# Optimization experiments

Measured on AMD Instinct MI355X. Metric: run time of the kernel, lower is better.

The kernel has to match this reference:

```python
import jax, jax.numpy as jnp
import numpy as np

EPS = 1e-7  # K.epsilon()

_LC = np.zeros((3, 3, 3), np.float32)  # Levi-Civita for 1x1->1
_LC[0, 1, 2] = _LC[1, 2, 0] = _LC[2, 0, 1] = 1.0
_LC[0, 2, 1] = _LC[2, 1, 0] = _LC[1, 0, 2] = -1.0


def _ssp(x):
    # shifted softplus: log(0.5*exp(x)+0.5)
    return jnp.log(0.5 * jnp.exp(x) + 0.5)


def _radial(image, w1, b1, w2, b2):
    # Sequential([Dense(32), Dense(feat)]) -- linear Dense layers (no activation)
    return (image @ w1 + b1) @ w2 + b2  # (m, a, b, feat)


def setup_inputs() -> dict:
    key = jax.random.key(0)
    ks = jax.random.split(key, 16)
    M, A, RBF, F, SI, H = 4, 256, 64, 32, 32, 32
    inp = {}
    inp["image"] = jax.random.uniform(ks[0], (M, A, A, RBF), dtype=jnp.float32)
    inp["vectors"] = jax.random.normal(ks[1], (M, A, A, 3), dtype=jnp.float32)
    inp["feat0"] = jax.random.normal(ks[2], (M, A, F, 1), dtype=jnp.float32)
    inp["feat1"] = jax.random.normal(ks[3], (M, A, F, 3), dtype=jnp.float32)
    i = 4
    for rin in (0, 1):
        for fro in (0, 1):
            tag = f"{rin}{fro}"
            inp[f"w1_{tag}"] = jax.random.normal(ks[i], (RBF, H)) / np.sqrt(RBF).astype(np.float32)
            inp[f"b1_{tag}"] = jnp.zeros((H,), jnp.float32)
            i += 1
            inp[f"w2_{tag}"] = jax.random.normal(ks[i], (H, F)) / np.sqrt(np.float32(H))
            inp[f"b2_{tag}"] = jnp.zeros((F,), jnp.float32)
            i += 1
    inp["w_si0"] = jax.random.normal(ks[i], (SI, 2 * F)) / np.sqrt(np.float32(2 * F)); i += 1
    inp["w_si1"] = jax.random.normal(ks[i], (SI, 3 * F)) / np.sqrt(np.float32(3 * F)); i += 1
    inp["b_act0"] = jnp.zeros((SI,), jnp.float32)
    inp["b_act1"] = jnp.zeros((SI,), jnp.float32)
    return inp


def reference(image, vectors, feat0, feat1,
              w1_00, b1_00, w2_00, b2_00,
              w1_01, b1_01, w2_01, b2_01,
              w1_10, b1_10, w2_10, b2_10,
              w1_11, b1_11, w2_11, b2_11,
              w_si0, w_si1, b_act0, b_act1):
    # mask where |r_ab| < eps (self-pairs / padding)
    mask = (jnp.sqrt(jnp.sum(vectors * vectors, axis=-1)) < EPS)[..., None]  # (m,a,b,1)

    def filt0(w1, b1, w2, b2):
        return _radial(image, w1, b1, w2, b2)  # (m,a,b,F), implicit rep index of size 1

    def filt1(w1, b1, w2, b2):
        r = jnp.where(mask, 0.0, _radial(image, w1, b1, w2, b2))  # masked radial
        return vectors[:, :, :, None, :] * r[..., None]  # (m,a,b,F,3)

    f0_in0 = filt0(w1_00, b1_00, w2_00, b2_00)
    f1_in0 = filt1(w1_01, b1_01, w2_01, b2_01)
    f0_in1 = filt0(w1_10, b1_10, w2_10, b2_10)
    f1_in1 = filt1(w1_11, b1_11, w2_11, b2_11)

    # point convolution (sum over neighbor atoms b)
    out_0x0_0 = jnp.einsum('mabf,mbfj->mafj', f0_in0, feat0)   # (m,a,F,1)
    out_0x1_1 = jnp.einsum('mabfi,mbfj->mafi', f1_in0, feat0)  # (m,a,F,3)
    out_1x0_1 = jnp.einsum('mabf,mbfj->mafj', f0_in1, feat1)   # (m,a,F,3)
    cg0 = jnp.eye(3, dtype=image.dtype)[None]                  # (1,3,3): 1x1->0
    out_1x1_0 = jnp.einsum('ijk,mabfj,mbfk->mafi', cg0, f1_in1, feat1)  # (m,a,F,1)
    lc = jnp.asarray(_LC, image.dtype)                         # 1x1->1
    out_1x1_1 = jnp.einsum('ijk,mabfj,mbfk->mafi', lc, f1_in1, feat1)   # (m,a,F,3)

    # concat along channel dim per output RO
    cat0 = jnp.concatenate([out_0x0_0, out_1x1_0], axis=2)  # (m,a,2F,1)
    cat1 = jnp.concatenate([out_0x1_1, out_1x0_1, out_1x1_1], axis=2)  # (m,a,3F,3)

    # self-interaction: einsum('mafi,gf->maig') then transpose -> (m,a,g,i)
    si0 = jnp.einsum('mafi,gf->magi', cat0, w_si0)  # (m,a,SI,1)
    si1 = jnp.einsum('mafi,gf->magi', cat1, w_si1)  # (m,a,SI,3)

    # equivariant activation
    o0 = _ssp(si0 + b_act0[None, None, :, None])
    n1 = jnp.sqrt(jnp.maximum(jnp.sum(si1 * si1, axis=-1), EPS))  # norm_with_epsilon
    a1 = _ssp(n1 + b_act1)
    o1 = si1 * (a1 / n1)[..., None]
    return (o0, o1)
```

## Files before the change

kernel.cpp:

```cpp
#include <hip/hip_runtime.h>
#include <math.h>

#define M_ 4
#define A_ 256
#define RBF_ 64
#define F_ 32
#define H_ 32
#define SI_ 32
#define TF_ 128

typedef __attribute__((ext_vector_type(8))) short bf16x8;
typedef __attribute__((ext_vector_type(4))) float f32x4;
typedef __attribute__((ext_vector_type(3))) float f32x3;

__device__ __forceinline__ unsigned short f2bf(float f) {
  union { float f; unsigned u; } v; v.f = f;
  unsigned r = v.u + 0x7FFFu + ((v.u >> 16) & 1u);
  return (unsigned short)(r >> 16);
}

__device__ __forceinline__ unsigned pack2bf(float lo, float hi) {
  union { float f; unsigned u; } a, b; a.f = lo; b.f = hi;
  return __builtin_amdgcn_perm(b.u + 0x8000u, a.u + 0x8000u, 0x07060302u);
}

__device__ __forceinline__ float sspf(float x) {
  return fmaxf(x, 0.f) + log1pf(expf(-fabsf(x))) - 0.6931471805599453f;
}

__global__ __launch_bounds__(256) void combine_weights(
    const float* __restrict__ w1_00, const float* __restrict__ b1_00,
    const float* __restrict__ w2_00, const float* __restrict__ b2_00,
    const float* __restrict__ w1_01, const float* __restrict__ b1_01,
    const float* __restrict__ w2_01, const float* __restrict__ b2_01,
    const float* __restrict__ w1_10, const float* __restrict__ b1_10,
    const float* __restrict__ w2_10, const float* __restrict__ b2_10,
    const float* __restrict__ w1_11, const float* __restrict__ b1_11,
    const float* __restrict__ w2_11, const float* __restrict__ b2_11,
    unsigned short* __restrict__ wsT, float* __restrict__ bcw)
{
  const float* w1s[4] = {w1_00, w1_01, w1_10, w1_11};
  const float* b1s[4] = {b1_00, b1_01, b1_10, b1_11};
  const float* w2s[4] = {w2_00, w2_01, w2_10, w2_11};
  const float* b2s[4] = {b2_00, b2_01, b2_10, b2_11};
  int tid = blockIdx.x * 256 + threadIdx.x;
  int k   = tid >> 7;
  int tf  = tid & 127;
  int tag = tf >> 5, f = tf & 31;
  const float* w1 = w1s[tag];
  const float* w2 = w2s[tag];
  float s = 0.f;
  for (int h = 0; h < H_; ++h) s += w1[k * H_ + h] * w2[h * F_ + f];
  wsT[tf * 64 + k] = f2bf(s);
  if (tid < TF_) {
    const float* b1 = b1s[tag];
    const float* b2 = b2s[tag];
    float sb = b2[f];
    for (int h = 0; h < H_; ++h) sb += b1[h] * w2[h * F_ + f];
    bcw[tf] = sb;
  }
}

__global__ __launch_bounds__(512, 4) void conv_fused(
    const float* __restrict__ image, const float* __restrict__ vectors,
    const float* __restrict__ feat0, const float* __restrict__ feat1,
    const unsigned short* __restrict__ wsT, const float* __restrict__ bcw,
    const float* __restrict__ w_si0, const float* __restrict__ w_si1,
    const float* __restrict__ b_act0, const float* __restrict__ b_act1,
    float* __restrict__ out)
{
  __shared__ __align__(16) unsigned short sA[2][32 * 72];
  __shared__ float sV[A_ * 3];
  __shared__ float cat[352];

  const int t    = threadIdx.x;
  const int ma   = blockIdx.x;
  const int m    = ma >> 8;
  const int l    = t & 63;
  const int n    = l & 15;
  const int quad = l >> 4;
  const int wu    = __builtin_amdgcn_readfirstlane(t >> 6);
  const int role  = (wu + ((ma & 3) << 1)) & 7;
  const int which = role & 1;
  const int tag   = role >> 1;
  const int ct    = tag * 2 + which;
  const int f     = which * 16 + n;

  const unsigned short* wr = wsT + (ct * 16 + n) * 64 + quad * 8;
  const bf16x8 w0 = *(const bf16x8*)(wr);
  const bf16x8 w1 = *(const bf16x8*)(wr + 32);
  const float  bc = bcw[ct * 16 + n];

  const int srow = t >> 4;
  const int scol = (t & 15) * 4;
  const float* gsrc = image + (size_t)ma * (A_ * RBF_) + srow * RBF_ + scol;
  unsigned short* sd0 = &sA[0][srow * 72 + scol];
  unsigned short* sd1 = &sA[1][srow * 72 + scol];

  float4 rE = *(const float4*)(gsrc);
  float4 rO = *(const float4*)(gsrc + 2048);
  gsrc += 4096;

  {
    const float* vsrc = vectors + (size_t)ma * (A_ * 3);
    sV[t] = vsrc[t];
    if (t < 256) sV[t + 512] = vsrc[t + 512];
  }

  const int b0q = quad * 4;
  const float* p0c = feat0 + (size_t)(m * A_ + b0q) * F_ + f;
  const float* p1c = feat1 + ((size_t)(m * A_ + b0q) * F_ + f) * 3;
  const float* svc = &sV[b0q * 3];
  const unsigned short* aB0 = &sA[0][n * 72 + quad * 8];
  const unsigned short* aB1 = &sA[1][n * 72 + quad * 8];

  float gx[2][4], gy[2][4], gz[2][4];
  float pA = 0.f, pB0 = 0.f, pB1 = 0.f, pB2 = 0.f;

#define PF(BUF) { \
    if (tag <= 1) { \
      _Pragma("unroll") \
      for (int r = 0; r < 4; ++r) gx[BUF][r] = p0c[r * F_]; \
    } else { \
      _Pragma("unroll") \
      for (int r = 0; r < 4; ++r) { \
        f32x3 v = *(const f32x3*)(p1c + r * (F_ * 3)); \
        gx[BUF][r] = v[0]; gy[BUF][r] = v[1]; gz[BUF][r] = v[2]; \
      } \
    } \
    p0c += 16 * F_; p1c += 16 * F_ * 3; }

#define BODY(AB, AOFF, SOFF, GX, GY, GZ) { \
    const bf16x8 a0 = *(const bf16x8*)(AB + (AOFF)); \
    const bf16x8 a1 = *(const bf16x8*)(AB + (AOFF) + 32); \
    f32x4 acc = {bc, bc, bc, bc}; \
    acc = __builtin_amdgcn_mfma_f32_16x16x32_bf16(a0, w0, acc, 0, 0, 0); \
    acc = __builtin_amdgcn_mfma_f32_16x16x32_bf16(a1, w1, acc, 0, 0, 0); \
    if (tag == 0) {             \
      _Pragma("unroll") \
      for (int r = 0; r < 4; ++r) pA += acc[r] * GX[r]; \
    } else if (tag == 1) {      \
      _Pragma("unroll") \
      for (int r = 0; r < 4; ++r) { \
        const float s = acc[r] * GX[r]; \
        pB0 += svc[(SOFF) + r * 3 + 0] * s; \
        pB1 += svc[(SOFF) + r * 3 + 1] * s; \
        pB2 += svc[(SOFF) + r * 3 + 2] * s; \
      } \
    } else if (tag == 2) {      \
      _Pragma("unroll") \
      for (int r = 0; r < 4; ++r) { \
        const float Rr = acc[r]; \
        pB0 += Rr * GX[r]; pB1 += Rr * GY[r]; pB2 += Rr * GZ[r]; \
      } \
    } else {                    \
      _Pragma("unroll") \
      for (int r = 0; r < 4; ++r) { \
        const float Rr = acc[r]; \
        const float ax = GX[r], ay = GY[r], az = GZ[r]; \
        const float vx = svc[(SOFF) + r * 3 + 0]; \
        const float vy = svc[(SOFF) + r * 3 + 1]; \
        const float vz = svc[(SOFF) + r * 3 + 2]; \
        float d = vx * ax; d = fmaf(vy, ay, d); d = fmaf(vz, az, d); \
        pA = fmaf(Rr, d, pA); \
        float c0 = vy * az; c0 = fmaf(-vz, ay, c0); pB0 = fmaf(Rr, c0, pB0); \
        float c1 = vz * ax; c1 = fmaf(-vx, az, c1); pB1 = fmaf(Rr, c1, pB1); \
        float c2 = vx * ay; c2 = fmaf(-vy, ax, c2); pB2 = fmaf(Rr, c2, pB2); \
      } \
    } }

#define BARRIER() { \
    asm volatile("s_waitcnt lgkmcnt(0)" ::: "memory"); \
    __builtin_amdgcn_s_barrier(); \
    asm volatile("" ::: "memory"); }

  PF(0)
  { uint2 pk; pk.x = pack2bf(rE.x, rE.y); pk.y = pack2bf(rE.z, rE.w);
    *(uint2*)sd0 = pk; }
  BARRIER();

  #pragma unroll 1
  for (int d = 0; d < 4; ++d) {
    if (d < 3) rE = *(const float4*)(gsrc);
    PF(1)
    BODY(aB0, 0, 0, gx[0], gy[0], gz[0])
    PF(0)
    BODY(aB0, 1152, 48, gx[1], gy[1], gz[1])
    { uint2 pk; pk.x = pack2bf(rO.x, rO.y); pk.y = pack2bf(rO.z, rO.w);
      *(uint2*)sd1 = pk; }
    BARRIER();
    if (d < 3) rO = *(const float4*)(gsrc + 2048);
    PF(1)
    BODY(aB1, 0, 96, gx[0], gy[0], gz[0])
    if (d < 3) PF(0)
    BODY(aB1, 1152, 144, gx[1], gy[1], gz[1])
    if (d < 3) {
      uint2 pk; pk.x = pack2bf(rE.x, rE.y); pk.y = pack2bf(rE.z, rE.w);
      *(uint2*)sd0 = pk;
      BARRIER();
    }
    gsrc += 4096;
    svc  += 192;
  }

#define QRED(x) { x += __shfl_xor(x, 16); x += __shfl_xor(x, 32); }
  QRED(pA) QRED(pB0) QRED(pB1) QRED(pB2)
  if (quad == 0) {
    if (tag == 0) {
      cat[f] = pA;
    } else if (tag == 1) {
      cat[64 + f * 3 + 0] = pB0; cat[64 + f * 3 + 1] = pB1; cat[64 + f * 3 + 2] = pB2;
    } else if (tag == 2) {
      cat[160 + f * 3 + 0] = pB0; cat[160 + f * 3 + 1] = pB1; cat[160 + f * 3 + 2] = pB2;
    } else {
      cat[32 + f] = pA;
      cat[256 + f * 3 + 0] = pB0; cat[256 + f * 3 + 1] = pB1; cat[256 + f * 3 + 2] = pB2;
    }
  }
  __syncthreads();

  if (t < 256) {
    const int g = t >> 3, p = t & 7;
    const float* wrow = w_si1 + g * 96 + p * 12;
    const float* c1 = &cat[64 + p * 36];
    float s0 = 0.f, s1 = 0.f, s2 = 0.f;
    #pragma unroll
    for (int k = 0; k < 12; ++k) {
      const float wv = wrow[k];
      s0 = fmaf(c1[k * 3 + 0], wv, s0);
      s1 = fmaf(c1[k * 3 + 1], wv, s1);
      s2 = fmaf(c1[k * 3 + 2], wv, s2);
    }
    s0 += __shfl_xor(s0, 1); s0 += __shfl_xor(s0, 2); s0 += __shfl_xor(s0, 4);
    s1 += __shfl_xor(s1, 1); s1 += __shfl_xor(s1, 2); s1 += __shfl_xor(s1, 4);
    s2 += __shfl_xor(s2, 1); s2 += __shfl_xor(s2, 2); s2 += __shfl_xor(s2, 4);
    if (p == 0) {
      const float n2 = s0 * s0 + s1 * s1 + s2 * s2;
      const float n1 = sqrtf(fmaxf(n2, 1e-7f));
      const float a1 = sspf(n1 + b_act1[g]);
      const float sc = a1 / n1;
      const int ob = M_ * A_ * SI_ + (ma * SI_ + g) * 3;
      out[ob + 0] = s0 * sc; out[ob + 1] = s1 * sc; out[ob + 2] = s2 * sc;
    }
  } else if (t < 320) {
    const int t2 = t - 256, g = t2 >> 1, p = t2 & 1;
    const float* wrow = w_si0 + g * 64 + p * 32;
    const float* c0 = &cat[p * 32];
    float s = 0.f;
    #pragma unroll 8
    for (int k = 0; k < 32; ++k) s = fmaf(c0[k], wrow[k], s);
    s += __shfl_xor(s, 1);
    if (p == 0) out[ma * SI_ + g] = sspf(s + b_act0[g]);
  }
}

extern "C" void kernel_launch(void* const* d_in, const int* in_sizes, int n_in,
                              void* d_out, int out_size, void* d_ws, size_t ws_size,
                              hipStream_t stream) {
  const float* image   = (const float*)d_in[0];
  const float* vectors = (const float*)d_in[1];
  const float* feat0   = (const float*)d_in[2];
  const float* feat1   = (const float*)d_in[3];
  const float* w_si0   = (const float*)d_in[20];
  const float* w_si1   = (const float*)d_in[21];
  const float* b_act0  = (const float*)d_in[22];
  const float* b_act1  = (const float*)d_in[23];
  unsigned short* wsT = (unsigned short*)d_ws;
  float* bcw  = (float*)((char*)d_ws + 16384);
  float* out  = (float*)d_out;

  combine_weights<<<32, 256, 0, stream>>>(
      (const float*)d_in[4],  (const float*)d_in[5],
      (const float*)d_in[6],  (const float*)d_in[7],
      (const float*)d_in[8],  (const float*)d_in[9],
      (const float*)d_in[10], (const float*)d_in[11],
      (const float*)d_in[12], (const float*)d_in[13],
      (const float*)d_in[14], (const float*)d_in[15],
      (const float*)d_in[16], (const float*)d_in[17],
      (const float*)d_in[18], (const float*)d_in[19],
      wsT, bcw);

  conv_fused<<<M_ * A_, 512, 0, stream>>>(
      image, vectors, feat0, feat1, wsT, bcw,
      w_si0, w_si1, b_act0, b_act1, out);
}
```

Measured before the change: 165.0 us.

## Stage whole image tile in LDS, cutting per-chunk barriers to one

Replaces the double-buffered 32-row image staging (a barrier every 32 rows) with a full 256-row bf16 tile in shared memory. The first half is loaded up front; the second half is streamed in during compute on the first half, so only one mid-kernel barrier is needed. The cat buffer now aliases sV, which requires an extra __syncthreads before the reduction writes. LDS use grows to about 37KB per block, which may cap occupancy below the four blocks per CU the launch bounds request.

```diff
diff --git a/kernel.cpp b/kernel.cpp
--- a/kernel.cpp
+++ b/kernel.cpp
@@ -69,9 +69,9 @@
     const float* __restrict__ b_act0, const float* __restrict__ b_act1,
     float* __restrict__ out)
 {
-  __shared__ __align__(16) unsigned short sA[2][32 * 72];
-  __shared__ float sV[A_ * 3];
-  __shared__ float cat[352];
+  __shared__ __align__(16) unsigned short sA[256 * 72];
+  __shared__ __align__(16) float sV[A_ * 3];
+  float* const cat = sV;
 
   const int t    = threadIdx.x;
   const int ma   = blockIdx.x;
@@ -91,28 +91,38 @@
   const bf16x8 w1 = *(const bf16x8*)(wr + 32);
   const float  bc = bcw[ct * 16 + n];
 
-  const int srow = t >> 4;
-  const int scol = (t & 15) * 4;
-  const float* gsrc = image + (size_t)ma * (A_ * RBF_) + srow * RBF_ + scol;
-  unsigned short* sd0 = &sA[0][srow * 72 + scol];
-  unsigned short* sd1 = &sA[1][srow * 72 + scol];
-
-  float4 rE = *(const float4*)(gsrc);
-  float4 rO = *(const float4*)(gsrc + 2048);
-  gsrc += 4096;
-
+  const int srow = t >> 2;
+  const int sc16 = (t & 3) << 4;
+  const float* g1 = image + (size_t)ma * (A_ * RBF_) + srow * RBF_ + sc16;
+  const float* g2 = g1 + 128 * RBF_;
+  unsigned short* w1p = &sA[srow * 72 + sc16];
+  unsigned short* w2p = &sA[(srow + 128) * 72 + sc16];
+
+  float4 a0 = *(const float4*)(g1);
+  float4 a1 = *(const float4*)(g1 + 4);
+  float4 a2 = *(const float4*)(g1 + 8);
+  float4 a3 = *(const float4*)(g1 + 12);
   {
     const float* vsrc = vectors + (size_t)ma * (A_ * 3);
     sV[t] = vsrc[t];
     if (t < 256) sV[t + 512] = vsrc[t + 512];
   }
+  {
+    uint4 pk;
+    pk.x = pack2bf(a0.x, a0.y); pk.y = pack2bf(a0.z, a0.w);
+    pk.z = pack2bf(a1.x, a1.y); pk.w = pack2bf(a1.z, a1.w);
+    *(uint4*)w1p = pk;
+    pk.x = pack2bf(a2.x, a2.y); pk.y = pack2bf(a2.z, a2.w);
+    pk.z = pack2bf(a3.x, a3.y); pk.w = pack2bf(a3.z, a3.w);
+    *(uint4*)(w1p + 8) = pk;
+  }
+  float4 hb = *(const float4*)(g2);
 
   const int b0q = quad * 4;
   const float* p0c = feat0 + (size_t)(m * A_ + b0q) * F_ + f;
   const float* p1c = feat1 + ((size_t)(m * A_ + b0q) * F_ + f) * 3;
   const float* svc = &sV[b0q * 3];
-  const unsigned short* aB0 = &sA[0][n * 72 + quad * 8];
-  const unsigned short* aB1 = &sA[1][n * 72 + quad * 8];
+  const unsigned short* aBc = &sA[n * 72 + quad * 8];
 
   float gx[2][4], gy[2][4], gz[2][4];
   float pA = 0.f, pB0 = 0.f, pB1 = 0.f, pB2 = 0.f;
@@ -130,12 +140,12 @@
     } \
     p0c += 16 * F_; p1c += 16 * F_ * 3; }
 
-#define BODY(AB, AOFF, SOFF, GX, GY, GZ) { \
-    const bf16x8 a0 = *(const bf16x8*)(AB + (AOFF)); \
-    const bf16x8 a1 = *(const bf16x8*)(AB + (AOFF) + 32); \
+#define BODY(AOFF, SOFF, GX, GY, GZ) { \
+    const bf16x8 a0_ = *(const bf16x8*)(aBc + (AOFF)); \
+    const bf16x8 a1_ = *(const bf16x8*)(aBc + (AOFF) + 32); \
     f32x4 acc = {bc, bc, bc, bc}; \
-    acc = __builtin_amdgcn_mfma_f32_16x16x32_bf16(a0, w0, acc, 0, 0, 0); \
-    acc = __builtin_amdgcn_mfma_f32_16x16x32_bf16(a1, w1, acc, 0, 0, 0); \
+    acc = __builtin_amdgcn_mfma_f32_16x16x32_bf16(a0_, w0, acc, 0, 0, 0); \
+    acc = __builtin_amdgcn_mfma_f32_16x16x32_bf16(a1_, w1, acc, 0, 0, 0); \
     if (tag == 0) {             \
       _Pragma("unroll") \
       for (int r = 0; r < 4; ++r) pA += acc[r] * GX[r]; \
@@ -175,36 +185,34 @@
     asm volatile("" ::: "memory"); }
 
   PF(0)
-  { uint2 pk; pk.x = pack2bf(rE.x, rE.y); pk.y = pack2bf(rE.z, rE.w);
-    *(uint2*)sd0 = pk; }
   BARRIER();
 
   #pragma unroll 1
   for (int d = 0; d < 4; ++d) {
-    if (d < 3) rE = *(const float4*)(gsrc);
     PF(1)
-    BODY(aB0, 0, 0, gx[0], gy[0], gz[0])
+    BODY(0, 0, gx[0], gy[0], gz[0])
     PF(0)
-    BODY(aB0, 1152, 48, gx[1], gy[1], gz[1])
-    { uint2 pk; pk.x = pack2bf(rO.x, rO.y); pk.y = pack2bf(rO.z, rO.w);
-      *(uint2*)sd1 = pk; }
-    BARRIER();
-    if (d < 3) rO = *(const float4*)(gsrc + 2048);
+    BODY(1152, 48, gx[1], gy[1], gz[1])
+    aBc += 2304; svc += 96;
+    { uint2 pk; pk.x = pack2bf(hb.x, hb.y); pk.y = pack2bf(hb.z, hb.w);
+      *(uint2*)w2p = pk; }
+    w2p += 4;
+    if (d < 3) { g2 += 4; hb = *(const float4*)(g2); }
+  }
+  BARRIER();
+
+  #pragma unroll 1
+  for (int d = 0; d < 4; ++d) {
     PF(1)
-    BODY(aB1, 0, 96, gx[0], gy[0], gz[0])
+    BODY(0, 0, gx[0], gy[0], gz[0])
     if (d < 3) PF(0)
-    BODY(aB1, 1152, 144, gx[1], gy[1], gz[1])
-    if (d < 3) {
-      uint2 pk; pk.x = pack2bf(rE.x, rE.y); pk.y = pack2bf(rE.z, rE.w);
-      *(uint2*)sd0 = pk;
-      BARRIER();
-    }
-    gsrc += 4096;
-    svc  += 192;
+    BODY(1152, 48, gx[1], gy[1], gz[1])
+    aBc += 2304; svc += 96;
   }
 
 #define QRED(x) { x += __shfl_xor(x, 16); x += __shfl_xor(x, 32); }
   QRED(pA) QRED(pB0) QRED(pB1) QRED(pB2)
+  __syncthreads();
   if (quad == 0) {
     if (tag == 0) {
       cat[f] = pA;
```

After: 158.8 us. 3.8% less time.
